# Kernel optimization log

Measured on AMD Instinct MI355X. Metric: run time of the kernel, lower is better.

The kernel has to match this reference:

```python
import jax, jax.numpy as jnp
import numpy as np

RADIUS = 3.0  # suppression radius in meters (init kwarg `radius`)


def _radius_nms(x, y, valid, radius):
    """Greedy radius NMS over points in index order.
    x, y: [N] coordinates; valid: [N] bool (point belongs to this class).
    Returns keep mask [N]: point kept iff valid and not within `radius` of
    any previously kept point.
    """
    N = x.shape[0]
    r2 = radius * radius

    def step(supp, i):
        keep = valid[i] & jnp.logical_not(supp[i])
        d2 = (x - x[i]) ** 2 + (y - y[i]) ** 2  # [N]
        supp = supp | (keep & (d2 <= r2))
        return supp, keep

    _, keeps = jax.lax.scan(step, jnp.zeros(N, dtype=bool), jnp.arange(N))
    return keeps


def setup_inputs() -> dict:
    key = jax.random.key(0)
    k1, k2 = jax.random.split(key)
    B, C, W, H, CL = 4, 4, 64, 128, 5
    segmented_channels = jax.random.normal(k1, (B, C, W, H), dtype=jnp.float32)
    # lidar channels 0,1 are x,y point coordinates (meters); scale for realism
    lidar = jax.random.normal(k2, (B, CL, W, H), dtype=jnp.float32) * 30.0
    return {"segmented_channels": segmented_channels, "lidar": lidar}


def reference(segmented_channels, lidar):
    B, C, W, H = segmented_channels.shape
    N = W * H
    # val, ind = segmented_channels.max(dim=1) -> per-pixel predicted class
    ind = jnp.argmax(segmented_channels, axis=1).reshape(B, N)  # [B, N] int
    x = lidar[:, 0].reshape(B, N)  # [B, N]
    y = lidar[:, 1].reshape(B, N)
    # classes 1 .. C-1 (class 0 = background, skipped in the loop)
    classes = jnp.arange(1, C)
    valid = ind[:, None, :] == classes[None, :, None]  # [B, C-1, N] bool
    # vmap greedy NMS over classes, then over batch (x,y shared across classes)
    nms_c = jax.vmap(_radius_nms, in_axes=(None, None, 0, None))
    nms_bc = jax.vmap(nms_c, in_axes=(0, 0, 0, None))
    keep = nms_bc(x, y, valid, RADIUS)  # [B, C-1, N] bool
    # dense (padded) stand-in for the ragged per-class kept point lists:
    # kept coordinates where keep, zeros elsewhere
    coords = jnp.stack([x, y], axis=-1)  # [B, N, 2]
    kept_coords = coords[:, None, :, :] * keep[..., None].astype(coords.dtype)  # [B, C-1, N, 2]
    return kept_coords, keep
```

## Files before the change

kernel.cpp:

```cpp
#include <hip/hip_runtime.h>
#include <cstdint>


#define NPTS 8192
#define CAP  2560
#define R2C  9.0f
#define GW   60
#define GORG 126.0f
#define GINV 0.23809524f
#define GMAXC 59.0f
#define GRPT 14

typedef unsigned long long u64;

__global__ __launch_bounds__(1024) void radius_nms_kernel(
    const float* __restrict__ seg,
    const float* __restrict__ lidar,
    float* __restrict__ out)
{
#pragma clang fp contract(off)
    const int bx   = blockIdx.x;
    const int b    = bx / 3;
    const int cls  = (bx % 3) + 1;
    const int tid  = threadIdx.x;
    const int lane = tid & 63;
    const int wv   = tid >> 6;

    __shared__ float2 xy[CAP + 1];
    __shared__ unsigned short oidx[CAP];
    __shared__ u64 keptW[CAP / 64];
    __shared__ int waveTot[16];
    __shared__ unsigned short slots[GW * GW * 4];
    __shared__ unsigned nib[(GW * GW + 7) / 8];
    __shared__ u64 adjT[GRPT * 64];

    float* out0 = out + (size_t)bx * NPTS * 2;
    float* out1 = out + 196608 + (size_t)bx * NPTS;

    {
        float4 z = make_float4(0.f, 0.f, 0.f, 0.f);
        float4* o0 = (float4*)out0;
        float4* o1 = (float4*)out1;
        for (int i = tid; i < NPTS / 2; i += 1024) o0[i] = z;
        for (int i = tid; i < NPTS / 4; i += 1024) o1[i] = z;
    }
    for (int i = tid; i < GW * GW * 2; i += 1024)
        ((unsigned*)slots)[i] = ((unsigned)CAP << 16) | (unsigned)CAP;
    for (int i = tid; i < (GW * GW + 7) / 8; i += 1024) nib[i] = 0u;
    if (tid == 0) xy[CAP] = make_float2(3.0e38f, 3.0e38f);
    if (tid < CAP / 64) keptW[tid] = 0ull;

    const float4* s4  = (const float4*)(seg + (size_t)b * 4 * NPTS);
    const float4* lx4 = (const float4*)(lidar + (size_t)b * 5 * NPTS);
    const float4* ly4 = lx4 + NPTS / 4;

    float px[8], py[8];
    int flags = 0, cnt = 0;
    const int n0 = tid * 8;
#pragma unroll
    for (int g = 0; g < 2; ++g) {
        const int vi = tid * 2 + g;
        float4 v0 = s4[vi];
        float4 v1 = s4[2048 + vi];
        float4 v2 = s4[4096 + vi];
        float4 v3 = s4[6144 + vi];
        float4 X  = lx4[vi];
        float4 Y  = ly4[vi];
#define ELT(FLD, E) { \
        int bi = 0; float bv = v0.FLD; \
        if (v1.FLD > bv) { bv = v1.FLD; bi = 1; } \
        if (v2.FLD > bv) { bv = v2.FLD; bi = 2; } \
        if (v3.FLD > bv) { bv = v3.FLD; bi = 3; } \
        px[g * 4 + E] = X.FLD; py[g * 4 + E] = Y.FLD; \
        if (bi == cls) { flags |= 1 << (g * 4 + E); ++cnt; } }
        ELT(x, 0) ELT(y, 1) ELT(z, 2) ELT(w, 3)
#undef ELT
    }

    int v = cnt;
    for (int off = 1; off < 64; off <<= 1) {
        int nv = __shfl_up(v, off, 64);
        if (lane >= off) v += nv;
    }
    if (lane == 63) waveTot[wv] = v;
    __syncthreads();
    if (wv == 0) {
        int t = (lane < 16) ? waveTot[lane] : 0;
        for (int off = 1; off < 16; off <<= 1) {
            int nt = __shfl_up(t, off, 64);
            if (lane >= off) t += nt;
        }
        if (lane < 16) waveTot[lane] = t;
    }
    __syncthreads();

    int M = waveTot[15];
    if (M > CAP) M = CAP;
    int base = ((wv == 0) ? 0 : waveTot[wv - 1]) + v - cnt;
#pragma unroll
    for (int k = 0; k < 8; ++k) {
        if ((flags >> k) & 1) {
            if (base < CAP) {
                xy[base] = make_float2(px[k], py[k]);
                oidx[base] = (unsigned short)(n0 + k);
            }
            ++base;
        }
    }
    __syncthreads();

    const int ntiles  = (M + 63) >> 6;
    const int ngroups = (ntiles + GRPT - 1) / GRPT;

    for (int g = 0; g < ngroups; ++g) {
        const int t0 = g * GRPT;

        if (wv >= 1 && wv <= GRPT) {
            const int t = t0 + wv - 1;
            if (t < ntiles) {
                const int ts = t << 6;
                const int p  = ts + lane;
                float2 q = xy[(p < M) ? p : CAP];
                u64 row = 0ull;
#pragma unroll
                for (int j = 0; j < 64; j += 2) {
                    float4 two = *(const float4*)&xy[ts + j];
                    float dx0 = q.x - two.x, dy0 = q.y - two.y;
                    float dx1 = q.x - two.z, dy1 = q.y - two.w;
                    float s0 = dx0 * dx0 + dy0 * dy0;
                    float s1 = dx1 * dx1 + dy1 * dy1;
                    row |= ((u64)(s0 <= R2C)) << j;
                    row |= ((u64)(s1 <= R2C)) << (j + 1);
                }
                adjT[(wv - 1) * 64 + lane] = row;
            }
        }
        __syncthreads();

        if (wv == 0) {
            const int tEnd = (t0 + GRPT < ntiles) ? t0 + GRPT : ntiles;
            int p0 = (t0 << 6) + lane;
            float2 qq = xy[(p0 < M) ? p0 : CAP];
            float qx = qq.x, qy = qq.y;
            int cx, cy;
            {
                float fx = floorf((qx + GORG) * GINV);
                fx = fminf(fmaxf(fx, 0.0f), GMAXC);
                float fy = floorf((qy + GORG) * GINV);
                fy = fminf(fmaxf(fy, 0.0f), GMAXC);
                cx = (int)fx; cy = (int)fy;
            }
            for (int t = t0; t < tEnd; ++t) {
                const int s  = t - t0;
                const int ts = t << 6;

                u64 row = adjT[s * 64 + lane];

                const int cxm = (cx > 0) ? cx - 1 : 0;
                const int cxp = (cx < GW - 1) ? cx + 1 : GW - 1;
                const int rm  = ((cy > 0) ? cy - 1 : 0) * GW;
                const int r0  = cy * GW;
                const int rp  = ((cy < GW - 1) ? cy + 1 : GW - 1) * GW;
                u64 sw[9];
                sw[0] = *(const u64*)&slots[(rm + cxm) * 4];
                sw[1] = *(const u64*)&slots[(rm + cx ) * 4];
                sw[2] = *(const u64*)&slots[(rm + cxp) * 4];
                sw[3] = *(const u64*)&slots[(r0 + cxm) * 4];
                sw[4] = *(const u64*)&slots[(r0 + cx ) * 4];
                sw[5] = *(const u64*)&slots[(r0 + cxp) * 4];
                sw[6] = *(const u64*)&slots[(rp + cxm) * 4];
                sw[7] = *(const u64*)&slots[(rp + cx ) * 4];
                sw[8] = *(const u64*)&slots[(rp + cxp) * 4];

                int pn = ((t + 1) << 6) + lane;
                float2 qn = xy[(pn < M) ? pn : CAP];

                float m = 1.0e30f;
#pragma unroll
                for (int w = 0; w < 9; ++w) {
                    u64 sww = sw[w];
#pragma unroll
                    for (int k = 0; k < 4; ++k) {
                        int idx = (int)((sww >> (16 * k)) & 0xFFFFull);
                        float2 r = xy[idx];
                        float dx = qx - r.x;
                        float dy = qy - r.y;
                        m = fminf(m, dx * dx + dy * dy);
                    }
                }
                const bool sup = (m <= R2C);

                int cntT = M - ts; if (cntT > 64) cntT = 64;
                u64 tm = (cntT >= 64) ? ~0ull : ((1ull << cntT) - 1ull);
                u64 alive = __ballot(!sup) & tm;
                u64 keepm = 0ull;
                const int rowLo = (int)(unsigned)row;
                const int rowHi = (int)(unsigned)(row >> 32);
                while (alive) {
                    const int l = __builtin_ctzll(alive);
                    unsigned rl = (unsigned)__builtin_amdgcn_readlane(rowLo, l);
                    unsigned rh = (unsigned)__builtin_amdgcn_readlane(rowHi, l);
                    keepm |= 1ull << l;
                    alive &= ~(((u64)rh << 32) | (u64)rl);
                }
                if (lane == 0) keptW[t] = keepm;

                if ((keepm >> lane) & 1ull) {
                    const int c = cy * GW + cx;
                    const unsigned sh = 4u * (unsigned)(c & 7);
                    unsigned old = atomicAdd(&nib[c >> 3], 1u << sh);
                    unsigned mc = (old >> sh) & 0xFu;
                    if (mc < 4u) slots[c * 4 + (int)mc] = (unsigned short)(ts + lane);
                }

                qx = qn.x; qy = qn.y;
                {
                    float fx = floorf((qx + GORG) * GINV);
                    fx = fminf(fmaxf(fx, 0.0f), GMAXC);
                    float fy = floorf((qy + GORG) * GINV);
                    fy = fminf(fmaxf(fy, 0.0f), GMAXC);
                    cx = (int)fx; cy = (int)fy;
                }
            }
        }
        __syncthreads();
    }

    for (int j = tid; j < M; j += 1024) {
        if ((keptW[j >> 6] >> (j & 63)) & 1ull) {
            const int n = oidx[j];
            float2 q = xy[j];
            out0[2 * n]     = q.x;
            out0[2 * n + 1] = q.y;
            out1[n]         = 1.0f;
        }
    }
}

extern "C" void kernel_launch(void* const* d_in, const int* in_sizes, int n_in,
                              void* d_out, int out_size, void* d_ws, size_t ws_size,
                              hipStream_t stream) {
    const float* seg   = (const float*)d_in[0];
    const float* lidar = (const float*)d_in[1];
    float* out = (float*)d_out;
    radius_nms_kernel<<<dim3(12), dim3(1024), 0, stream>>>(seg, lidar, out);
}
```

Baseline: 124.4 us.

## Replace serial tile-wise greedy NMS with parallel cell-sorted iterative resolution

```diff
diff --git a/kernel.cpp b/kernel.cpp
--- a/kernel.cpp
+++ b/kernel.cpp
@@ -6,12 +6,20 @@
 #define CAP  2560
 #define R2C  9.0f
 #define GW   60
+#define NC   (GW * GW)
 #define GORG 126.0f
 #define GINV 0.23809524f
 #define GMAXC 59.0f
-#define GRPT 14
 
 typedef unsigned long long u64;
+
+__device__ __forceinline__ void cell_of(float X, float Y, int& cx, int& cy) {
+    float fx = floorf((X + GORG) * GINV);
+    fx = fminf(fmaxf(fx, 0.0f), GMAXC);
+    float fy = floorf((Y + GORG) * GINV);
+    fy = fminf(fmaxf(fy, 0.0f), GMAXC);
+    cx = (int)fx; cy = (int)fy;
+}
 
 __global__ __launch_bounds__(1024) void radius_nms_kernel(
     const float* __restrict__ seg,
@@ -26,13 +34,11 @@
     const int lane = tid & 63;
     const int wv   = tid >> 6;
 
-    __shared__ float2 xy[CAP + 1];
-    __shared__ unsigned short oidx[CAP];
-    __shared__ u64 keptW[CAP / 64];
+    __shared__ float2 cellXY[CAP];
+    __shared__ unsigned short cellPix[CAP];
+    __shared__ volatile unsigned char status[CAP];
+    __shared__ unsigned cellOff[NC];
     __shared__ int waveTot[16];
-    __shared__ unsigned short slots[GW * GW * 4];
-    __shared__ unsigned nib[(GW * GW + 7) / 8];
-    __shared__ u64 adjT[GRPT * 64];
 
     float* out0 = out + (size_t)bx * NPTS * 2;
     float* out1 = out + 196608 + (size_t)bx * NPTS;
@@ -44,18 +50,15 @@
         for (int i = tid; i < NPTS / 2; i += 1024) o0[i] = z;
         for (int i = tid; i < NPTS / 4; i += 1024) o1[i] = z;
     }
-    for (int i = tid; i < GW * GW * 2; i += 1024)
-        ((unsigned*)slots)[i] = ((unsigned)CAP << 16) | (unsigned)CAP;
-    for (int i = tid; i < (GW * GW + 7) / 8; i += 1024) nib[i] = 0u;
-    if (tid == 0) xy[CAP] = make_float2(3.0e38f, 3.0e38f);
-    if (tid < CAP / 64) keptW[tid] = 0ull;
+    for (int i = tid; i < NC; i += 1024) cellOff[i] = 0u;
+    for (int i = tid; i < CAP; i += 1024) status[i] = 0;
 
     const float4* s4  = (const float4*)(seg + (size_t)b * 4 * NPTS);
     const float4* lx4 = (const float4*)(lidar + (size_t)b * 5 * NPTS);
     const float4* ly4 = lx4 + NPTS / 4;
 
     float px[8], py[8];
-    int flags = 0, cnt = 0;
+    int flags = 0;
     const int n0 = tid * 8;
 #pragma unroll
     for (int g = 0; g < 2; ++g) {
@@ -72,12 +75,31 @@
         if (v2.FLD > bv) { bv = v2.FLD; bi = 2; } \
         if (v3.FLD > bv) { bv = v3.FLD; bi = 3; } \
         px[g * 4 + E] = X.FLD; py[g * 4 + E] = Y.FLD; \
-        if (bi == cls) { flags |= 1 << (g * 4 + E); ++cnt; } }
+        if (bi == cls) flags |= 1 << (g * 4 + E); }
         ELT(x, 0) ELT(y, 1) ELT(z, 2) ELT(w, 3)
 #undef ELT
     }
-
-    int v = cnt;
+    __syncthreads();
+
+#pragma unroll
+    for (int k = 0; k < 8; ++k) {
+        if ((flags >> k) & 1) {
+            int cx, cy;
+            cell_of(px[k], py[k], cx, cy);
+            atomicAdd(&cellOff[cy * GW + cx], 1u);
+        }
+    }
+    __syncthreads();
+
+    unsigned c0 = 0, c1 = 0, c2 = 0, c3 = 0, sum = 0;
+    if (tid < NC / 4) {
+        c0 = cellOff[4 * tid];
+        c1 = cellOff[4 * tid + 1];
+        c2 = cellOff[4 * tid + 2];
+        c3 = cellOff[4 * tid + 3];
+        sum = c0 + c1 + c2 + c3;
+    }
+    int v = (int)sum;
     for (int off = 1; off < 64; off <<= 1) {
         int nv = __shfl_up(v, off, 64);
         if (lane >= off) v += nv;
@@ -93,145 +115,108 @@
         if (lane < 16) waveTot[lane] = t;
     }
     __syncthreads();
-
     int M = waveTot[15];
     if (M > CAP) M = CAP;
-    int base = ((wv == 0) ? 0 : waveTot[wv - 1]) + v - cnt;
+    if (tid < NC / 4) {
+        unsigned excl = (unsigned)(((wv == 0) ? 0 : waveTot[wv - 1]) + v - (int)sum);
+        cellOff[4 * tid]     = excl;
+        cellOff[4 * tid + 1] = excl + c0;
+        cellOff[4 * tid + 2] = excl + c0 + c1;
+        cellOff[4 * tid + 3] = excl + c0 + c1 + c2;
+    }
+    __syncthreads();
+
 #pragma unroll
     for (int k = 0; k < 8; ++k) {
         if ((flags >> k) & 1) {
-            if (base < CAP) {
-                xy[base] = make_float2(px[k], py[k]);
-                oidx[base] = (unsigned short)(n0 + k);
+            int cx, cy;
+            cell_of(px[k], py[k], cx, cy);
+            unsigned pos = atomicAdd(&cellOff[cy * GW + cx], 1u);
+            if (pos < CAP) {
+                cellXY[pos]  = make_float2(px[k], py[k]);
+                cellPix[pos] = (unsigned short)(n0 + k);
             }
-            ++base;
-        }
-    }
-    __syncthreads();
-
-    const int ntiles  = (M + 63) >> 6;
-    const int ngroups = (ntiles + GRPT - 1) / GRPT;
-
-    for (int g = 0; g < ngroups; ++g) {
-        const int t0 = g * GRPT;
-
-        if (wv >= 1 && wv <= GRPT) {
-            const int t = t0 + wv - 1;
-            if (t < ntiles) {
-                const int ts = t << 6;
-                const int p  = ts + lane;
-                float2 q = xy[(p < M) ? p : CAP];
-                u64 row = 0ull;
-#pragma unroll
-                for (int j = 0; j < 64; j += 2) {
-                    float4 two = *(const float4*)&xy[ts + j];
-                    float dx0 = q.x - two.x, dy0 = q.y - two.y;
-                    float dx1 = q.x - two.z, dy1 = q.y - two.w;
-                    float s0 = dx0 * dx0 + dy0 * dy0;
-                    float s1 = dx1 * dx1 + dy1 * dy1;
-                    row |= ((u64)(s0 <= R2C)) << j;
-                    row |= ((u64)(s1 <= R2C)) << (j + 1);
+        }
+    }
+    __syncthreads();
+
+    float    qx[3], qy[3];
+    unsigned pix[3];
+    unsigned lo[3][3], hi[3][3];
+    bool     keepF[3] = {false, false, false};
+    unsigned rem = 0;
+#pragma unroll
+    for (int s = 0; s < 3; ++s) {
+        const int q = tid + s * 1024;
+        if (q < M) {
+            float2 p = cellXY[q];
+            qx[s] = p.x; qy[s] = p.y;
+            pix[s] = cellPix[q];
+            int cx, cy;
+            cell_of(p.x, p.y, cx, cy);
+            const int cxm = (cx > 0) ? cx - 1 : 0;
+            const int cxp = (cx < GW - 1) ? cx + 1 : GW - 1;
+            const int ry0 = (cy > 0) ? cy - 1 : 0;
+            const int ry1 = (cy < GW - 1) ? cy + 1 : GW - 1;
+#pragma unroll
+            for (int r = 0; r < 3; ++r) {
+                const int rr = ry0 + r;
+                if (rr <= ry1) {
+                    const int a  = rr * GW + cxm;
+                    const int bb = rr * GW + cxp;
+                    unsigned l = (a == 0) ? 0u : cellOff[a - 1];
+                    unsigned h = cellOff[bb];
+                    lo[s][r] = (l < (unsigned)M) ? l : (unsigned)M;
+                    hi[s][r] = (h < (unsigned)M) ? h : (unsigned)M;
+                } else {
+                    lo[s][r] = 0u; hi[s][r] = 0u;
                 }
-                adjT[(wv - 1) * 64 + lane] = row;
             }
-        }
-        __syncthreads();
-
-        if (wv == 0) {
-            const int tEnd = (t0 + GRPT < ntiles) ? t0 + GRPT : ntiles;
-            int p0 = (t0 << 6) + lane;
-            float2 qq = xy[(p0 < M) ? p0 : CAP];
-            float qx = qq.x, qy = qq.y;
-            int cx, cy;
-            {
-                float fx = floorf((qx + GORG) * GINV);
-                fx = fminf(fmaxf(fx, 0.0f), GMAXC);
-                float fy = floorf((qy + GORG) * GINV);
-                fy = fminf(fmaxf(fy, 0.0f), GMAXC);
-                cx = (int)fx; cy = (int)fy;
-            }
-            for (int t = t0; t < tEnd; ++t) {
-                const int s  = t - t0;
-                const int ts = t << 6;
-
-                u64 row = adjT[s * 64 + lane];
-
-                const int cxm = (cx > 0) ? cx - 1 : 0;
-                const int cxp = (cx < GW - 1) ? cx + 1 : GW - 1;
-                const int rm  = ((cy > 0) ? cy - 1 : 0) * GW;
-                const int r0  = cy * GW;
-                const int rp  = ((cy < GW - 1) ? cy + 1 : GW - 1) * GW;
-                u64 sw[9];
-                sw[0] = *(const u64*)&slots[(rm + cxm) * 4];
-                sw[1] = *(const u64*)&slots[(rm + cx ) * 4];
-                sw[2] = *(const u64*)&slots[(rm + cxp) * 4];
-                sw[3] = *(const u64*)&slots[(r0 + cxm) * 4];
-                sw[4] = *(const u64*)&slots[(r0 + cx ) * 4];
-                sw[5] = *(const u64*)&slots[(r0 + cxp) * 4];
-                sw[6] = *(const u64*)&slots[(rp + cxm) * 4];
-                sw[7] = *(const u64*)&slots[(rp + cx ) * 4];
-                sw[8] = *(const u64*)&slots[(rp + cxp) * 4];
-
-                int pn = ((t + 1) << 6) + lane;
-                float2 qn = xy[(pn < M) ? pn : CAP];
-
-                float m = 1.0e30f;
-#pragma unroll
-                for (int w = 0; w < 9; ++w) {
-                    u64 sww = sw[w];
-#pragma unroll
-                    for (int k = 0; k < 4; ++k) {
-                        int idx = (int)((sww >> (16 * k)) & 0xFFFFull);
-                        float2 r = xy[idx];
-                        float dx = qx - r.x;
-                        float dy = qy - r.y;
-                        m = fminf(m, dx * dx + dy * dy);
+            rem |= 1u << s;
+        } else {
+            qx[s] = 0.f; qy[s] = 0.f; pix[s] = 0;
+#pragma unroll
+            for (int r = 0; r < 3; ++r) { lo[s][r] = 0u; hi[s][r] = 0u; }
+        }
+    }
+
+    while (rem) {
+#pragma unroll
+        for (int s = 0; s < 3; ++s) {
+            if (rem & (1u << s)) {
+                bool sawKept = false, hasUnk = false;
+#pragma unroll
+                for (int r = 0; r < 3; ++r) {
+                    for (unsigned j = lo[s][r]; j < hi[s][r]; ++j) {
+                        float2 rp = cellXY[j];
+                        float dx = qx[s] - rp.x;
+                        float dy = qy[s] - rp.y;
+                        if (dx * dx + dy * dy <= R2C) {
+                            unsigned pj = cellPix[j];
+                            if (pj < pix[s]) {
+                                unsigned char st = status[j];
+                                sawKept |= (st == 1);
+                                hasUnk  |= (st == 0);
+                            }
+                        }
                     }
                 }
-                const bool sup = (m <= R2C);
-
-                int cntT = M - ts; if (cntT > 64) cntT = 64;
-                u64 tm = (cntT >= 64) ? ~0ull : ((1ull << cntT) - 1ull);
-                u64 alive = __ballot(!sup) & tm;
-                u64 keepm = 0ull;
-                const int rowLo = (int)(unsigned)row;
-                const int rowHi = (int)(unsigned)(row >> 32);
-                while (alive) {
-                    const int l = __builtin_ctzll(alive);
-                    unsigned rl = (unsigned)__builtin_amdgcn_readlane(rowLo, l);
-                    unsigned rh = (unsigned)__builtin_amdgcn_readlane(rowHi, l);
-                    keepm |= 1ull << l;
-                    alive &= ~(((u64)rh << 32) | (u64)rl);
-                }
-                if (lane == 0) keptW[t] = keepm;
-
-                if ((keepm >> lane) & 1ull) {
-                    const int c = cy * GW + cx;
-                    const unsigned sh = 4u * (unsigned)(c & 7);
-                    unsigned old = atomicAdd(&nib[c >> 3], 1u << sh);
-                    unsigned mc = (old >> sh) & 0xFu;
-                    if (mc < 4u) slots[c * 4 + (int)mc] = (unsigned short)(ts + lane);
-                }
-
-                qx = qn.x; qy = qn.y;
-                {
-                    float fx = floorf((qx + GORG) * GINV);
-                    fx = fminf(fmaxf(fx, 0.0f), GMAXC);
-                    float fy = floorf((qy + GORG) * GINV);
-                    fy = fminf(fmaxf(fy, 0.0f), GMAXC);
-                    cx = (int)fx; cy = (int)fy;
+                const int q = tid + s * 1024;
+                if (sawKept) {
+                    status[q] = 2; rem &= ~(1u << s);
+                } else if (!hasUnk) {
+                    status[q] = 1; keepF[s] = true; rem &= ~(1u << s);
                 }
             }
         }
-        __syncthreads();
-    }
-
-    for (int j = tid; j < M; j += 1024) {
-        if ((keptW[j >> 6] >> (j & 63)) & 1ull) {
-            const int n = oidx[j];
-            float2 q = xy[j];
-            out0[2 * n]     = q.x;
-            out0[2 * n + 1] = q.y;
+    }
+
+#pragma unroll
+    for (int s = 0; s < 3; ++s) {
+        if (keepF[s]) {
+            const int n = (int)pix[s];
+            out0[2 * n]     = qx[s];
+            out0[2 * n + 1] = qy[s];
             out1[n]         = 1.0f;
         }
     }
```

Result: slower. 210.7 us (+69.3%).

## Replace spatial-grid NMS with wave-pipelined kept-list scan via shared ctrl word

Applied to the files above, without the earlier changes.

```diff
diff --git a/kernel.cpp b/kernel.cpp
--- a/kernel.cpp
+++ b/kernel.cpp
@@ -5,11 +5,7 @@
 #define NPTS 8192
 #define CAP  2560
 #define R2C  9.0f
-#define GW   60
-#define GORG 126.0f
-#define GINV 0.23809524f
-#define GMAXC 59.0f
-#define GRPT 14
+#define NW   16
 
 typedef unsigned long long u64;
 
@@ -27,12 +23,11 @@
     const int wv   = tid >> 6;
 
     __shared__ float2 xy[CAP + 1];
+    __shared__ float2 kxy[CAP];
     __shared__ unsigned short oidx[CAP];
     __shared__ u64 keptW[CAP / 64];
     __shared__ int waveTot[16];
-    __shared__ unsigned short slots[GW * GW * 4];
-    __shared__ unsigned nib[(GW * GW + 7) / 8];
-    __shared__ u64 adjT[GRPT * 64];
+    __shared__ volatile unsigned ctrl;
 
     float* out0 = out + (size_t)bx * NPTS * 2;
     float* out1 = out + 196608 + (size_t)bx * NPTS;
@@ -44,11 +39,7 @@
         for (int i = tid; i < NPTS / 2; i += 1024) o0[i] = z;
         for (int i = tid; i < NPTS / 4; i += 1024) o1[i] = z;
     }
-    for (int i = tid; i < GW * GW * 2; i += 1024)
-        ((unsigned*)slots)[i] = ((unsigned)CAP << 16) | (unsigned)CAP;
-    for (int i = tid; i < (GW * GW + 7) / 8; i += 1024) nib[i] = 0u;
-    if (tid == 0) xy[CAP] = make_float2(3.0e38f, 3.0e38f);
-    if (tid < CAP / 64) keptW[tid] = 0ull;
+    if (tid == 0) { xy[CAP] = make_float2(3.0e38f, 3.0e38f); ctrl = 0u; }
 
     const float4* s4  = (const float4*)(seg + (size_t)b * 4 * NPTS);
     const float4* lx4 = (const float4*)(lidar + (size_t)b * 5 * NPTS);
@@ -109,122 +100,73 @@
     }
     __syncthreads();
 
-    const int ntiles  = (M + 63) >> 6;
-    const int ngroups = (ntiles + GRPT - 1) / GRPT;
+    const int ntiles = (M + 63) >> 6;
+    for (int t = wv; t < ntiles; t += NW) {
+        const int ts = t << 6;
+        const int p  = ts + lane;
+        float2 q = xy[(p < M) ? p : CAP];
 
-    for (int g = 0; g < ngroups; ++g) {
-        const int t0 = g * GRPT;
+        u64 row = 0ull;
+#pragma unroll
+        for (int j = 0; j < 64; j += 2) {
+            float4 two = *(const float4*)&xy[ts + j];
+            float dx0 = q.x - two.x, dy0 = q.y - two.y;
+            float dx1 = q.x - two.z, dy1 = q.y - two.w;
+            row |= ((u64)((dx0 * dx0 + dy0 * dy0) <= R2C)) << j;
+            row |= ((u64)((dx1 * dx1 + dy1 * dy1) <= R2C)) << (j + 1);
+        }
 
-        if (wv >= 1 && wv <= GRPT) {
-            const int t = t0 + wv - 1;
-            if (t < ntiles) {
-                const int ts = t << 6;
-                const int p  = ts + lane;
-                float2 q = xy[(p < M) ? p : CAP];
-                u64 row = 0ull;
-#pragma unroll
-                for (int j = 0; j < 64; j += 2) {
-                    float4 two = *(const float4*)&xy[ts + j];
-                    float dx0 = q.x - two.x, dy0 = q.y - two.y;
-                    float dx1 = q.x - two.z, dy1 = q.y - two.w;
-                    float s0 = dx0 * dx0 + dy0 * dy0;
-                    float s1 = dx1 * dx1 + dy1 * dy1;
-                    row |= ((u64)(s0 <= R2C)) << j;
-                    row |= ((u64)(s1 <= R2C)) << (j + 1);
-                }
-                adjT[(wv - 1) * 64 + lane] = row;
+        float m = 1.0e30f;
+        unsigned scanned = 0;
+        unsigned c;
+        for (;;) {
+            c = ctrl;
+            const unsigned nk = c & 0xFFFFu;
+            while (scanned + 2 <= nk) {
+                float2 k0 = kxy[scanned];
+                float2 k1 = kxy[scanned + 1];
+                float dx0 = q.x - k0.x, dy0 = q.y - k0.y;
+                float dx1 = q.x - k1.x, dy1 = q.y - k1.y;
+                m = fminf(m, dx0 * dx0 + dy0 * dy0);
+                m = fminf(m, dx1 * dx1 + dy1 * dy1);
+                scanned += 2;
             }
+            if (scanned < nk) {
+                float2 k0 = kxy[scanned];
+                float dx0 = q.x - k0.x, dy0 = q.y - k0.y;
+                m = fminf(m, dx0 * dx0 + dy0 * dy0);
+                ++scanned;
+            }
+            if ((c >> 16) >= (unsigned)t) break;
+            __builtin_amdgcn_s_sleep(1);
         }
-        __syncthreads();
+        const unsigned nk = c & 0xFFFFu;
 
-        if (wv == 0) {
-            const int tEnd = (t0 + GRPT < ntiles) ? t0 + GRPT : ntiles;
-            int p0 = (t0 << 6) + lane;
-            float2 qq = xy[(p0 < M) ? p0 : CAP];
-            float qx = qq.x, qy = qq.y;
-            int cx, cy;
-            {
-                float fx = floorf((qx + GORG) * GINV);
-                fx = fminf(fmaxf(fx, 0.0f), GMAXC);
-                float fy = floorf((qy + GORG) * GINV);
-                fy = fminf(fmaxf(fy, 0.0f), GMAXC);
-                cx = (int)fx; cy = (int)fy;
-            }
-            for (int t = t0; t < tEnd; ++t) {
-                const int s  = t - t0;
-                const int ts = t << 6;
+        const bool sup = (m <= R2C);
+        int cntT = M - ts; if (cntT > 64) cntT = 64;
+        u64 tm = (cntT >= 64) ? ~0ull : ((1ull << cntT) - 1ull);
+        u64 alive = __ballot(!sup) & tm;
+        u64 keepm = 0ull;
+        const int rowLo = (int)(unsigned)row;
+        const int rowHi = (int)(unsigned)(row >> 32);
+        while (alive) {
+            const int l = __builtin_ctzll(alive);
+            unsigned rl = (unsigned)__builtin_amdgcn_readlane(rowLo, l);
+            unsigned rh = (unsigned)__builtin_amdgcn_readlane(rowHi, l);
+            keepm |= 1ull << l;
+            alive &= ~(((u64)rh << 32) | (u64)rl);
+        }
+        if (lane == 0) keptW[t] = keepm;
 
-                u64 row = adjT[s * 64 + lane];
-
-                const int cxm = (cx > 0) ? cx - 1 : 0;
-                const int cxp = (cx < GW - 1) ? cx + 1 : GW - 1;
-                const int rm  = ((cy > 0) ? cy - 1 : 0) * GW;
-                const int r0  = cy * GW;
-                const int rp  = ((cy < GW - 1) ? cy + 1 : GW - 1) * GW;
-                u64 sw[9];
-                sw[0] = *(const u64*)&slots[(rm + cxm) * 4];
-                sw[1] = *(const u64*)&slots[(rm + cx ) * 4];
-                sw[2] = *(const u64*)&slots[(rm + cxp) * 4];
-                sw[3] = *(const u64*)&slots[(r0 + cxm) * 4];
-                sw[4] = *(const u64*)&slots[(r0 + cx ) * 4];
-                sw[5] = *(const u64*)&slots[(r0 + cxp) * 4];
-                sw[6] = *(const u64*)&slots[(rp + cxm) * 4];
-                sw[7] = *(const u64*)&slots[(rp + cx ) * 4];
-                sw[8] = *(const u64*)&slots[(rp + cxp) * 4];
-
-                int pn = ((t + 1) << 6) + lane;
-                float2 qn = xy[(pn < M) ? pn : CAP];
-
-                float m = 1.0e30f;
-#pragma unroll
-                for (int w = 0; w < 9; ++w) {
-                    u64 sww = sw[w];
-#pragma unroll
-                    for (int k = 0; k < 4; ++k) {
-                        int idx = (int)((sww >> (16 * k)) & 0xFFFFull);
-                        float2 r = xy[idx];
-                        float dx = qx - r.x;
-                        float dy = qy - r.y;
-                        m = fminf(m, dx * dx + dy * dy);
-                    }
-                }
-                const bool sup = (m <= R2C);
-
-                int cntT = M - ts; if (cntT > 64) cntT = 64;
-                u64 tm = (cntT >= 64) ? ~0ull : ((1ull << cntT) - 1ull);
-                u64 alive = __ballot(!sup) & tm;
-                u64 keepm = 0ull;
-                const int rowLo = (int)(unsigned)row;
-                const int rowHi = (int)(unsigned)(row >> 32);
-                while (alive) {
-                    const int l = __builtin_ctzll(alive);
-                    unsigned rl = (unsigned)__builtin_amdgcn_readlane(rowLo, l);
-                    unsigned rh = (unsigned)__builtin_amdgcn_readlane(rowHi, l);
-                    keepm |= 1ull << l;
-                    alive &= ~(((u64)rh << 32) | (u64)rl);
-                }
-                if (lane == 0) keptW[t] = keepm;
-
-                if ((keepm >> lane) & 1ull) {
-                    const int c = cy * GW + cx;
-                    const unsigned sh = 4u * (unsigned)(c & 7);
-                    unsigned old = atomicAdd(&nib[c >> 3], 1u << sh);
-                    unsigned mc = (old >> sh) & 0xFu;
-                    if (mc < 4u) slots[c * 4 + (int)mc] = (unsigned short)(ts + lane);
-                }
-
-                qx = qn.x; qy = qn.y;
-                {
-                    float fx = floorf((qx + GORG) * GINV);
-                    fx = fminf(fmaxf(fx, 0.0f), GMAXC);
-                    float fy = floorf((qy + GORG) * GINV);
-                    fy = fminf(fmaxf(fy, 0.0f), GMAXC);
-                    cx = (int)fx; cy = (int)fy;
-                }
-            }
-        }
-        __syncthreads();
+        const int nkept = __popcll(keepm);
+        const unsigned pos =
+            nk + (unsigned)__popcll(keepm & ((1ull << lane) - 1ull));
+        if ((keepm >> lane) & 1ull) kxy[pos] = q;
+        __threadfence_block();
+        if (lane == 0)
+            ctrl = ((unsigned)(t + 1) << 16) | (nk + (unsigned)nkept);
     }
+    __syncthreads();
 
     for (int j = tid; j < M; j += 1024) {
         if ((keptW[j >> 6] >> (j & 63)) & 1ull) {
```

Result: slower. 209.1 us (+68.1%).
